# Performance work log

Measured on AMD Instinct MI355X. Metric: run time of the kernel, lower is better.

Reference implementation:

```python
import jax, jax.numpy as jnp
import numpy as np

B_SZ, SEQ, H, P = 4, 8192, 512, 256


def _s5(x, lam_re, lam_im, log_dt, b_re, b_im, c_re, c_im, d):
    """Single-direction S5 diagonal SSM. x: [B,L,H] -> y: [B,L,H]."""
    lam = lam_re + 1j * lam_im                      # [P] complex diagonal A
    dt = jnp.exp(log_dt)                            # [P] ZOH timestep
    a_bar = jnp.exp(lam * dt)                       # [P] discretized A
    b_bar = ((a_bar - 1.0) / lam)[:, None] * (b_re + 1j * b_im)  # [P,H]
    bu = jnp.einsum('blh,ph->blp', x.astype(b_bar.dtype), b_bar)  # [B,L,P]
    a_el = jnp.broadcast_to(a_bar, bu.shape)        # time-invariant A per step

    def comb(e1, e2):  # associative combine for linear recurrence
        a1, s1 = e1
        a2, s2 = e2
        return (a1 * a2, a2 * s1 + s2)

    _, states = jax.lax.associative_scan(comb, (a_el, bu), axis=1)  # [B,L,P]
    c = c_re + 1j * c_im                            # [H,P]
    return jnp.einsum('blp,hp->blh', states, c).real + x * d


def setup_inputs() -> dict:
    key = jax.random.key(0)
    ks = jax.random.split(key, 10)
    return {
        'x': jax.random.normal(ks[0], (B_SZ, SEQ, H), dtype=jnp.float32),
        'Lambda_re': -0.1 - 0.5 * jax.random.uniform(ks[1], (2, P), dtype=jnp.float32),
        'Lambda_im': jnp.pi * jax.random.normal(ks[2], (2, P), dtype=jnp.float32),
        'log_dt': jnp.log(0.001) + (jnp.log(0.1) - jnp.log(0.001)) * jax.random.uniform(ks[3], (2, P), dtype=jnp.float32),
        'B_re': jax.random.normal(ks[4], (2, P, H), dtype=jnp.float32) / np.sqrt(H),
        'B_im': jax.random.normal(ks[5], (2, P, H), dtype=jnp.float32) / np.sqrt(H),
        'C_re': jax.random.normal(ks[6], (2, H, P), dtype=jnp.float32) / np.sqrt(P),
        'C_im': jax.random.normal(ks[7], (2, H, P), dtype=jnp.float32) / np.sqrt(P),
        'D': jax.random.normal(ks[8], (2, H), dtype=jnp.float32),
    }


def reference(x, Lambda_re, Lambda_im, log_dt, B_re, B_im, C_re, C_im, D):
    # fwd(x) + flip(bwd(flip(x)))
    y_f = _s5(x, Lambda_re[0], Lambda_im[0], log_dt[0], B_re[0], B_im[0], C_re[0], C_im[0], D[0])
    x_r = x[:, ::-1]
    y_b = _s5(x_r, Lambda_re[1], Lambda_im[1], log_dt[1], B_re[1], B_im[1], C_re[1], C_im[1], D[1])[:, ::-1]
    return y_f + y_b
```

## Files before the change

kernel.cpp:

```cpp
#include <hip/hip_runtime.h>
#include <math.h>

typedef unsigned short ushort_t;
typedef __bf16 bf16x8 __attribute__((ext_vector_type(8)));
typedef ushort_t ushort8v __attribute__((ext_vector_type(8)));
typedef float f32x4 __attribute__((ext_vector_type(4)));

#define B_SZ   4
#define SEQ    8192
#define M_ROWS (B_SZ * SEQ)
#define CH     128
#define NC     (SEQ / CH)

__device__ __forceinline__ ushort_t f2bf(float f) {
    unsigned u = __float_as_uint(f);
    u = u + 0x7fffu + ((u >> 16) & 1u);
    return (ushort_t)(u >> 16);
}
__device__ __forceinline__ float bf2f(ushort_t b) {
    return __uint_as_float(((unsigned)b) << 16);
}

__device__ __forceinline__ void load16_lds(const void* g, void* l) {
    __builtin_amdgcn_global_load_lds(
        (const __attribute__((address_space(1))) unsigned int*)g,
        (__attribute__((address_space(3))) unsigned int*)l, 16, 0, 0);
}

__device__ __forceinline__ bf16x8 ldfrag(const ushort_t* p) {
    union { ushort8v u; bf16x8 b; } cv;
    cv.u = *(const ushort8v*)p;
    return cv.b;
}

__device__ __forceinline__ float2 cmul(float2 a, float2 b) {
    return make_float2(a.x * b.x - a.y * b.y, a.x * b.y + a.y * b.x);
}

__global__ void prepconv_kernel(const float* __restrict__ x,
                                ushort_t* __restrict__ X16,
                                const float* __restrict__ Lre,
                                const float* __restrict__ Lim,
                                const float* __restrict__ ldt,
                                const float* __restrict__ Bre,
                                const float* __restrict__ Bim,
                                const float* __restrict__ Cre,
                                const float* __restrict__ Cim,
                                float* __restrict__ abar,
                                float* __restrict__ apow,
                                float* __restrict__ PW,
                                ushort_t* __restrict__ Bmat,
                                ushort_t* __restrict__ Cmat) {
    int i = blockIdx.x * 256 + threadIdx.x;
    float4 v = ((const float4*)x)[i];
    ushort_t o[4] = {f2bf(v.x), f2bf(v.y), f2bf(v.z), f2bf(v.w)};
    *(uint2*)&X16[(size_t)i * 4] = *(const uint2*)o;

    if (blockIdx.x < 1024) {
        int idx = i;
        int h = idx & 511;
        int p = (idx >> 9) & 255;
        int d = idx >> 17;
        int ip = d * 256 + p;
        float lr = Lre[ip], li = Lim[ip];
        float dt = expf(ldt[ip]);
        float e   = expf(lr * dt);
        float ang = li * dt;
        float ar = e * cosf(ang), ai = e * sinf(ang);
        float nr = ar - 1.0f, ni = ai;
        float den = lr * lr + li * li;
        float cr = (nr * lr + ni * li) / den;
        float ci = (ni * lr - nr * li) / den;
        float br = Bre[idx], bi = Bim[idx];
        Bmat[(d * 512 + 2 * p) * 512 + h]     = f2bf(cr * br - ci * bi);
        Bmat[(d * 512 + 2 * p + 1) * 512 + h] = f2bf(cr * bi + ci * br);
        if (h == 0) {
            int oo = d * 512 + 2 * p;
            abar[oo] = ar;  abar[oo + 1] = ai;
            float eC = expf(lr * dt * (float)CH);
            float aC = ang * (float)CH;
            apow[oo] = eC * cosf(aC);  apow[oo + 1] = eC * sinf(aC);
            float2 a1 = make_float2(ar, ai);
            float2 a2 = cmul(a1, a1);
            float2 a4 = cmul(a2, a2);
            float2 a8 = cmul(a4, a4);
            float2 a16 = cmul(a8, a8);
            float2 a32 = cmul(a16, a16);
            float2 a64 = cmul(a32, a32);
            int q = d * 256 + p;
            PW[q * 8 + 0] = a1.x;  PW[q * 8 + 1] = a1.y;
            PW[q * 8 + 2] = a4.x;  PW[q * 8 + 3] = a4.y;
            PW[q * 8 + 4] = a16.x; PW[q * 8 + 5] = a16.y;
            PW[q * 8 + 6] = a64.x; PW[q * 8 + 7] = a64.y;
        }
        int p2 = idx & 255;
        int h2 = (idx >> 8) & 511;
        int d2 = idx >> 17;
        Cmat[h2 * 1024 + d2 * 512 + 2 * p2]     = f2bf(Cre[idx]);
        Cmat[h2 * 1024 + d2 * 512 + 2 * p2 + 1] = f2bf(-Cim[idx]);
    }
}

template<int EPI, int KD_, int NT>
__global__ __launch_bounds__(512, 4)
void gemm_bk32(const ushort_t* __restrict__ A, const ushort_t* __restrict__ Bm,
               ushort_t* __restrict__ Cb, float* __restrict__ Cf,
               const float* __restrict__ X, const float* __restrict__ Dv,
               const float* __restrict__ PW, float* __restrict__ CAR) {
    __shared__ char smem[49152];
    ushort_t (*shA)[4096] = (ushort_t(*)[4096])smem;
    ushort_t (*shB)[8192] = (ushort_t(*)[8192])(smem + 16384);
    constexpr int NKT = KD_ / 32;

    const int tid  = threadIdx.x;
    const int lane = tid & 63;
    const int wv   = tid >> 6;
    const int wr = wv >> 2, wc = wv & 3;
    const int l15 = lane & 15, lq = lane >> 4;

    const int lin = blockIdx.x;
    const int xcd = lin & 7;
    const int j   = lin >> 3;
    const int mt  = xcd * 32 + j / NT;
    const int nt  = j % NT;
    const int m0 = mt * 128;
    const int n0 = nt * 256;
    const int CN = NT * 256;

    f32x4 acc[4][4];
#pragma unroll
    for (int i = 0; i < 4; ++i)
#pragma unroll
        for (int jj = 0; jj < 4; ++jj)
            acc[i][jj] = (f32x4){0.f, 0.f, 0.f, 0.f};

    const int srA = wv * 16 + (lane >> 2);
    const int srB = wv * 32 + (lane >> 2);
    const int sck = (((lane & 3) ^ ((lane >> 3) & 3))) * 8;
    const ushort_t* Ag = A  + (size_t)(m0 + srA) * KD_ + sck;
    const ushort_t* Bg = Bm + (size_t)(n0 + srB) * KD_ + sck;

#define STAGE(t) do {                                                         \
        load16_lds(Ag + (size_t)(t) * 32, &shA[(t) & 1][wv * 512]);           \
        load16_lds(Bg + (size_t)(t) * 32, &shB[(t) & 1][wv * 1024]);          \
        load16_lds(Bg + (size_t)(t) * 32 + (size_t)16 * KD_,                  \
                   &shB[(t) & 1][wv * 1024 + 512]);                           \
    } while (0)

    const int rdoff = ((lq ^ ((l15 >> 1) & 3))) * 8;
    const int rdA = (wr * 64 + l15) * 32 + rdoff;
    const int rdB = (wc * 64 + l15) * 32 + rdoff;

    STAGE(0); STAGE(1);
    asm volatile("s_waitcnt vmcnt(3)" ::: "memory");
    __builtin_amdgcn_s_barrier();

#pragma unroll 2
    for (int kt = 0; kt < NKT; ++kt) {
        const int buf = kt & 1;
        bf16x8 af[4], bq[4];
#pragma unroll
        for (int mi = 0; mi < 4; ++mi)
            af[mi] = ldfrag(&shA[buf][rdA + mi * 512]);
#pragma unroll
        for (int ni = 0; ni < 4; ++ni)
            bq[ni] = ldfrag(&shB[buf][rdB + ni * 512]);
        __builtin_amdgcn_s_barrier();
        if (kt + 2 < NKT) STAGE(kt + 2);
        __builtin_amdgcn_s_setprio(1);
#pragma unroll
        for (int mi = 0; mi < 4; ++mi)
#pragma unroll
            for (int ni = 0; ni < 4; ++ni)
                acc[mi][ni] = __builtin_amdgcn_mfma_f32_16x16x32_bf16(
                    af[mi], bq[ni], acc[mi][ni], 0, 0, 0);
        __builtin_amdgcn_s_setprio(0);
        if (kt + 1 < NKT) {
            if (kt + 2 < NKT)
                asm volatile("s_waitcnt vmcnt(3)" ::: "memory");
            else
                asm volatile("s_waitcnt vmcnt(0)" ::: "memory");
            __builtin_amdgcn_s_barrier();
        }
    }
#undef STAGE

    asm volatile("s_waitcnt lgkmcnt(0)" ::: "memory");
    __builtin_amdgcn_s_barrier();

    const int rr = lane >> 2;
    const int cc = (lane & 3) * 16;

    if (EPI == 0) {
        ushort_t* ep = (ushort_t*)(smem + wv * 2304);
#pragma unroll
        for (int mi = 0; mi < 4; ++mi) {
#pragma unroll
            for (int ni = 0; ni < 4; ++ni)
#pragma unroll
                for (int r = 0; r < 4; ++r)
                    ep[(lq * 4 + r) * 72 + ni * 16 + l15] = f2bf(acc[mi][ni][r]);
            uint4 w0 = *(const uint4*)&ep[rr * 72 + cc];
            uint4 w1 = *(const uint4*)&ep[rr * 72 + cc + 8];
            const int rowg = m0 + wr * 64 + mi * 16 + rr;
            *(uint4*)&Cb[(size_t)rowg * CN + n0 + wc * 64 + cc]     = w0;
            *(uint4*)&Cb[(size_t)rowg * CN + n0 + wc * 64 + cc + 8] = w1;
        }
    } else {
        float* epf = (float*)(smem + wv * 4352);
        const int colbase = n0 + wc * 64 + cc;
        f32x4 dsv[4];
#pragma unroll
        for (int j4 = 0; j4 < 4; ++j4)
            dsv[j4] = *(const f32x4*)&Dv[colbase + j4 * 4]
                    + *(const f32x4*)&Dv[512 + colbase + j4 * 4];
#pragma unroll
        for (int mi = 0; mi < 4; ++mi) {
#pragma unroll
            for (int ni = 0; ni < 4; ++ni)
#pragma unroll
                for (int r = 0; r < 4; ++r)
                    epf[(lq * 4 + r) * 68 + ni * 16 + l15] = acc[mi][ni][r];
            const int rowg = m0 + wr * 64 + mi * 16 + rr;
            const size_t gb = (size_t)rowg * 512 + colbase;
#pragma unroll
            for (int j4 = 0; j4 < 4; ++j4) {
                f32x4 v  = *(const f32x4*)&epf[rr * 68 + cc + j4 * 4];
                f32x4 xv = *(const f32x4*)&X[gb + j4 * 4];
                v = v + xv * dsv[j4];
                *(f32x4*)&Cf[gb + j4 * 4] = v;
            }
        }
    }

    if (EPI == 0) {
        float* PLDS = (float*)(smem + 20480);
        const int dirq = ((n0 + wc * 64) >> 9) & 1;
        const bool evn = ((l15 & 1) == 0);
        float csA[4], cpA[4], a64x[4], a64y[4];

#define CACC(MI, R, CCo) do {                                                 \
            float vo = bf2f(f2bf(acc[MI][ni][R]));                            \
            float vp = __shfl_xor(vo, 1);                                     \
            float vr = evn ? vo : vp;                                         \
            float vi = evn ? vp : vo;                                         \
            wr_ = fmaf(CCo.x, vr, fmaf(-CCo.y, vi, wr_));                     \
            wi_ = fmaf(CCo.x, vi, fmaf(CCo.y, vr, wi_));                      \
        } while (0)
#define CSTEP(MI) do {                                                        \
            float wr_ = 0.f, wi_ = 0.f;                                       \
            CACC(MI, 0, c0); CACC(MI, 1, c1);                                 \
            CACC(MI, 2, c2); CACC(MI, 3, c3);                                 \
            float comp = evn ? (t16.x * wr_ - t16.y * wi_)                    \
                             : (t16.x * wi_ + t16.y * wr_);                   \
            csum += comp;                                                     \
            t16 = cmul(t16, A16);                                             \
        } while (0)

#pragma unroll
        for (int ni = 0; ni < 4; ++ni) {
            const int col = n0 + wc * 64 + ni * 16 + l15;
            const int q = col >> 1;
            float2 A1  = make_float2(PW[q * 8 + 0], PW[q * 8 + 1]);
            float2 A4  = make_float2(PW[q * 8 + 2], PW[q * 8 + 3]);
            float2 A16 = make_float2(PW[q * 8 + 4], PW[q * 8 + 5]);
            a64x[ni] = PW[q * 8 + 6]; a64y[ni] = PW[q * 8 + 7];
            const int lqp = dirq ? lq : 3 - lq;
            float2 A4_2 = cmul(A4, A4);
            float2 A4_3 = cmul(A4_2, A4);
            float2 P4 = (lqp == 0) ? make_float2(1.f, 0.f)
                       : (lqp == 1) ? A4
                       : (lqp == 2) ? A4_2 : A4_3;
            float2 c0, c1, c2, c3;
            if (dirq == 0) {
                c3 = P4; c2 = cmul(c3, A1); c1 = cmul(c2, A1); c0 = cmul(c1, A1);
            } else {
                c0 = P4; c1 = cmul(c0, A1); c2 = cmul(c1, A1); c3 = cmul(c2, A1);
            }
            float2 t16 = make_float2(1.f, 0.f);
            float csum = 0.f;
            if (dirq == 0) { CSTEP(3); CSTEP(2); CSTEP(1); CSTEP(0); }
            else           { CSTEP(0); CSTEP(1); CSTEP(2); CSTEP(3); }
            csum += __shfl_xor(csum, 16);
            csum += __shfl_xor(csum, 32);
            csA[ni] = csum;
            cpA[ni] = __shfl_xor(csum, 1);
            if (lq == 0)
                PLDS[wr * 256 + wc * 64 + ni * 16 + l15] = csum;
        }
        __builtin_amdgcn_s_barrier();
        if (wr == 0) {
#pragma unroll
            for (int ni = 0; ni < 4; ++ni) {
                const int cl = wc * 64 + ni * 16 + l15;
                float oth_same = PLDS[256 + cl];
                float oth_part = PLDS[256 + (cl ^ 1)];
                float own_re = evn ? csA[ni] : cpA[ni];
                float own_im = evn ? cpA[ni] : csA[ni];
                float oth_re = evn ? oth_same : oth_part;
                float oth_im = evn ? oth_part : oth_same;
                float Xre = dirq ? oth_re : own_re;
                float Xim = dirq ? oth_im : own_im;
                float Ysm = dirq ? csA[ni] : oth_same;
                float out = evn
                    ? fmaf(a64x[ni], Xre, fmaf(-a64y[ni], Xim, Ysm))
                    : fmaf(a64x[ni], Xim, fmaf( a64y[ni], Xre, Ysm));
                if (lq == 0)
                    CAR[(size_t)(m0 >> 7) * 1024 + n0 + cl] = out;
            }
        }
#undef CACC
#undef CSTEP
    }
}

__global__ __launch_bounds__(512)
void scan_fin2(ushort_t* __restrict__ S, const float* __restrict__ abar,
               const float* __restrict__ apow, const float* __restrict__ carry) {
    int b = blockIdx.x, c = blockIdx.y, t = threadIdx.x;
    int dir = t >> 8, p = t & 255;
    float ar = abar[dir * 512 + 2 * p], ai = abar[dir * 512 + 2 * p + 1];
    float pr = apow[dir * 512 + 2 * p], pi = apow[dir * 512 + 2 * p + 1];
    float sr = 0.f, si = 0.f;
    if (dir == 0) {
        for (int cc = 0; cc < c; ++cc) {
            int o = (b * NC + cc) * 1024 + 2 * p;
            float cr0 = carry[o], ci0 = carry[o + 1];
            float nr = fmaf(pr, sr, fmaf(-pi, si, cr0));
            float ni = fmaf(pr, si, fmaf(pi, sr, ci0));
            sr = nr; si = ni;
        }
    } else {
        for (int cc = NC - 1; cc > c; --cc) {
            int o = (b * NC + cc) * 1024 + 512 + 2 * p;
            float cr0 = carry[o], ci0 = carry[o + 1];
            float nr = fmaf(pr, sr, fmaf(-pi, si, cr0));
            float ni = fmaf(pr, si, fmaf(pi, sr, ci0));
            sr = nr; si = ni;
        }
    }
    ushort_t* base = S + ((size_t)b * SEQ + (size_t)c * CH) * 1024
                       + dir * 512 + 2 * p;
    for (int ii = 0; ii < CH; ++ii) {
        int i = dir ? (CH - 1 - ii) : ii;
        unsigned* addr = (unsigned*)(base + (size_t)i * 1024);
        unsigned u = *addr;
        float re = bf2f((ushort_t)(u & 0xffffu));
        float im = bf2f((ushort_t)(u >> 16));
        float nr = fmaf(ar, sr, fmaf(-ai, si, re));
        float ni = fmaf(ar, si, fmaf(ai, sr, im));
        sr = nr; si = ni;
        *addr = ((unsigned)f2bf(si) << 16) | (unsigned)f2bf(sr);
    }
}

extern "C" void kernel_launch(void* const* d_in, const int* in_sizes, int n_in,
                              void* d_out, int out_size, void* d_ws, size_t ws_size,
                              hipStream_t stream) {
    const float* x   = (const float*)d_in[0];
    const float* Lre = (const float*)d_in[1];
    const float* Lim = (const float*)d_in[2];
    const float* ldt = (const float*)d_in[3];
    const float* Bre = (const float*)d_in[4];
    const float* Bim = (const float*)d_in[5];
    const float* Cre = (const float*)d_in[6];
    const float* Cim = (const float*)d_in[7];
    const float* Dv  = (const float*)d_in[8];
    float* y = (float*)d_out;
    char* ws = (char*)d_ws;

    ushort_t* SB16 = (ushort_t*)(ws);
    ushort_t* X16  = (ushort_t*)(ws + 67108864);
    ushort_t* Bm16 = (ushort_t*)(ws + 100663296);
    ushort_t* Cm16 = (ushort_t*)(ws + 101711872);
    float* abar  = (float*)(ws + 102760448);
    float* apow  = (float*)(ws + 102764544);
    float* carry = (float*)d_out;
    float* PW    = (float*)((char*)d_out + 1048576);

    prepconv_kernel<<<16384, 256, 0, stream>>>(x, X16, Lre, Lim, ldt,
                                               Bre, Bim, Cre, Cim,
                                               abar, apow, PW, Bm16, Cm16);

    gemm_bk32<0, 512, 4><<<1024, 512, 0, stream>>>(X16, Bm16, SB16, nullptr,
                                                   nullptr, nullptr, PW, carry);

    dim3 gs(B_SZ, NC);
    scan_fin2<<<gs, 512, 0, stream>>>(SB16, abar, apow, carry);

    gemm_bk32<1, 1024, 2><<<512, 512, 0, stream>>>(SB16, Cm16, nullptr, y,
                                                   x, Dv, nullptr, nullptr);
}
```

Measured before the change: 279.8 us.

## Fuse x bf16 conversion into GEMM1 and fuse scan fixup into GEMM2

Drops the separate x-to-bf16 pass: GEMM1 now loads fp32 x from global, converts it in registers and writes it to LDS. Per-64-row chunk carries are emitted straight from GEMM1 without the cross-warp combine. A new kernel, one block per 64-row chunk, serially accumulates the carries, applies the intra-chunk scan in registers, stores the states to LDS and runs the C projection GEMM there with the D skip term. This removes the X16 round trip, the in-place scan's read-modify-write of SB, and one launch. The cost is a long serial carry loop per block (up to 127 steps), a 160KB LDS footprint that allows only one block per CU, and A-tile conversion work added to GEMM1.

```diff
diff --git a/kernel.cpp b/kernel.cpp
--- a/kernel.cpp
+++ b/kernel.cpp
@@ -37,80 +37,65 @@
     return make_float2(a.x * b.x - a.y * b.y, a.x * b.y + a.y * b.x);
 }
 
-__global__ void prepconv_kernel(const float* __restrict__ x,
-                                ushort_t* __restrict__ X16,
-                                const float* __restrict__ Lre,
-                                const float* __restrict__ Lim,
-                                const float* __restrict__ ldt,
-                                const float* __restrict__ Bre,
-                                const float* __restrict__ Bim,
-                                const float* __restrict__ Cre,
-                                const float* __restrict__ Cim,
-                                float* __restrict__ abar,
-                                float* __restrict__ apow,
-                                float* __restrict__ PW,
-                                ushort_t* __restrict__ Bmat,
-                                ushort_t* __restrict__ Cmat) {
-    int i = blockIdx.x * 256 + threadIdx.x;
-    float4 v = ((const float4*)x)[i];
-    ushort_t o[4] = {f2bf(v.x), f2bf(v.y), f2bf(v.z), f2bf(v.w)};
-    *(uint2*)&X16[(size_t)i * 4] = *(const uint2*)o;
-
-    if (blockIdx.x < 1024) {
-        int idx = i;
-        int h = idx & 511;
-        int p = (idx >> 9) & 255;
-        int d = idx >> 17;
-        int ip = d * 256 + p;
-        float lr = Lre[ip], li = Lim[ip];
-        float dt = expf(ldt[ip]);
-        float e   = expf(lr * dt);
-        float ang = li * dt;
-        float ar = e * cosf(ang), ai = e * sinf(ang);
-        float nr = ar - 1.0f, ni = ai;
-        float den = lr * lr + li * li;
-        float cr = (nr * lr + ni * li) / den;
-        float ci = (ni * lr - nr * li) / den;
-        float br = Bre[idx], bi = Bim[idx];
-        Bmat[(d * 512 + 2 * p) * 512 + h]     = f2bf(cr * br - ci * bi);
-        Bmat[(d * 512 + 2 * p + 1) * 512 + h] = f2bf(cr * bi + ci * br);
-        if (h == 0) {
-            int oo = d * 512 + 2 * p;
-            abar[oo] = ar;  abar[oo + 1] = ai;
-            float eC = expf(lr * dt * (float)CH);
-            float aC = ang * (float)CH;
-            apow[oo] = eC * cosf(aC);  apow[oo + 1] = eC * sinf(aC);
-            float2 a1 = make_float2(ar, ai);
-            float2 a2 = cmul(a1, a1);
-            float2 a4 = cmul(a2, a2);
-            float2 a8 = cmul(a4, a4);
-            float2 a16 = cmul(a8, a8);
-            float2 a32 = cmul(a16, a16);
-            float2 a64 = cmul(a32, a32);
-            int q = d * 256 + p;
-            PW[q * 8 + 0] = a1.x;  PW[q * 8 + 1] = a1.y;
-            PW[q * 8 + 2] = a4.x;  PW[q * 8 + 3] = a4.y;
-            PW[q * 8 + 4] = a16.x; PW[q * 8 + 5] = a16.y;
-            PW[q * 8 + 6] = a64.x; PW[q * 8 + 7] = a64.y;
-        }
-        int p2 = idx & 255;
-        int h2 = (idx >> 8) & 511;
-        int d2 = idx >> 17;
-        Cmat[h2 * 1024 + d2 * 512 + 2 * p2]     = f2bf(Cre[idx]);
-        Cmat[h2 * 1024 + d2 * 512 + 2 * p2 + 1] = f2bf(-Cim[idx]);
-    }
-}
-
-template<int EPI, int KD_, int NT>
+__global__ void prep_kernel(const float* __restrict__ Lre,
+                            const float* __restrict__ Lim,
+                            const float* __restrict__ ldt,
+                            const float* __restrict__ Bre,
+                            const float* __restrict__ Bim,
+                            const float* __restrict__ Cre,
+                            const float* __restrict__ Cim,
+                            float* __restrict__ abar,
+                            float* __restrict__ PW,
+                            ushort_t* __restrict__ Bmat,
+                            ushort_t* __restrict__ Cmat) {
+    int idx = blockIdx.x * 256 + threadIdx.x;
+    int h = idx & 511;
+    int p = (idx >> 9) & 255;
+    int d = idx >> 17;
+    int ip = d * 256 + p;
+    float lr = Lre[ip], li = Lim[ip];
+    float dt = expf(ldt[ip]);
+    float e   = expf(lr * dt);
+    float ang = li * dt;
+    float ar = e * cosf(ang), ai = e * sinf(ang);
+    float nr = ar - 1.0f, ni = ai;
+    float den = lr * lr + li * li;
+    float cr = (nr * lr + ni * li) / den;
+    float ci = (ni * lr - nr * li) / den;
+    float br = Bre[idx], bi = Bim[idx];
+    Bmat[(d * 512 + 2 * p) * 512 + h]     = f2bf(cr * br - ci * bi);
+    Bmat[(d * 512 + 2 * p + 1) * 512 + h] = f2bf(cr * bi + ci * br);
+    if (h == 0) {
+        int oo = d * 512 + 2 * p;
+        abar[oo] = ar;  abar[oo + 1] = ai;
+        float2 a1 = make_float2(ar, ai);
+        float2 a2 = cmul(a1, a1);
+        float2 a4 = cmul(a2, a2);
+        float2 a8 = cmul(a4, a4);
+        float2 a16 = cmul(a8, a8);
+        float2 a32 = cmul(a16, a16);
+        float2 a64 = cmul(a32, a32);
+        int q = d * 256 + p;
+        PW[q * 8 + 0] = a1.x;  PW[q * 8 + 1] = a1.y;
+        PW[q * 8 + 2] = a4.x;  PW[q * 8 + 3] = a4.y;
+        PW[q * 8 + 4] = a16.x; PW[q * 8 + 5] = a16.y;
+        PW[q * 8 + 6] = a64.x; PW[q * 8 + 7] = a64.y;
+    }
+    int p2 = idx & 255;
+    int h2 = (idx >> 8) & 511;
+    int d2 = idx >> 17;
+    Cmat[h2 * 1024 + d2 * 512 + 2 * p2]     = f2bf(Cre[idx]);
+    Cmat[h2 * 1024 + d2 * 512 + 2 * p2 + 1] = f2bf(-Cim[idx]);
+}
+
 __global__ __launch_bounds__(512, 4)
-void gemm_bk32(const ushort_t* __restrict__ A, const ushort_t* __restrict__ Bm,
-               ushort_t* __restrict__ Cb, float* __restrict__ Cf,
-               const float* __restrict__ X, const float* __restrict__ Dv,
-               const float* __restrict__ PW, float* __restrict__ CAR) {
+void gemm1_kernel(const float* __restrict__ Xf, const ushort_t* __restrict__ Bm,
+                  ushort_t* __restrict__ Cb, const float* __restrict__ PW,
+                  float* __restrict__ CAR) {
     __shared__ char smem[49152];
     ushort_t (*shA)[4096] = (ushort_t(*)[4096])smem;
     ushort_t (*shB)[8192] = (ushort_t(*)[8192])(smem + 16384);
-    constexpr int NKT = KD_ / 32;
+    constexpr int KD_ = 512, NT = 4, NKT = 16;
 
     const int tid  = threadIdx.x;
     const int lane = tid & 63;
@@ -134,14 +119,25 @@
         for (int jj = 0; jj < 4; ++jj)
             acc[i][jj] = (f32x4){0.f, 0.f, 0.f, 0.f};
 
-    const int srA = wv * 16 + (lane >> 2);
+    const int arow = tid >> 2;
+    const int ac   = tid & 3;
+    const float* Axg = Xf + (size_t)(m0 + arow) * KD_ + ac * 8;
+    const int awoff = arow * 64 + ((ac ^ ((arow >> 1) & 3)) * 16);
+
     const int srB = wv * 32 + (lane >> 2);
     const int sck = (((lane & 3) ^ ((lane >> 3) & 3))) * 8;
-    const ushort_t* Ag = A  + (size_t)(m0 + srA) * KD_ + sck;
     const ushort_t* Bg = Bm + (size_t)(n0 + srB) * KD_ + sck;
 
-#define STAGE(t) do {                                                         \
-        load16_lds(Ag + (size_t)(t) * 32, &shA[(t) & 1][wv * 512]);           \
+    float4 aLo, aHi;
+#define GLB_A(t) do { aLo = *(const float4*)(Axg + (size_t)(t) * 32);         \
+                      aHi = *(const float4*)(Axg + (size_t)(t) * 32 + 4);     \
+                 } while (0)
+#define WRITE_A(t) do {                                                       \
+        ushort_t tmp[8] = {f2bf(aLo.x), f2bf(aLo.y), f2bf(aLo.z), f2bf(aLo.w),\
+                           f2bf(aHi.x), f2bf(aHi.y), f2bf(aHi.z), f2bf(aHi.w)};\
+        *(uint4*)((char*)&shA[(t) & 1][0] + awoff) = *(const uint4*)tmp;      \
+    } while (0)
+#define STAGE_B(t) do {                                                       \
         load16_lds(Bg + (size_t)(t) * 32, &shB[(t) & 1][wv * 1024]);          \
         load16_lds(Bg + (size_t)(t) * 32 + (size_t)16 * KD_,                  \
                    &shB[(t) & 1][wv * 1024 + 512]);                           \
@@ -151,8 +147,11 @@
     const int rdA = (wr * 64 + l15) * 32 + rdoff;
     const int rdB = (wc * 64 + l15) * 32 + rdoff;
 
-    STAGE(0); STAGE(1);
-    asm volatile("s_waitcnt vmcnt(3)" ::: "memory");
+    GLB_A(0);
+    STAGE_B(0); STAGE_B(1);
+    WRITE_A(0);
+    asm volatile("s_waitcnt vmcnt(2)" ::: "memory");
+    asm volatile("s_waitcnt lgkmcnt(0)" ::: "memory");
     __builtin_amdgcn_s_barrier();
 
 #pragma unroll 2
@@ -165,8 +164,13 @@
 #pragma unroll
         for (int ni = 0; ni < 4; ++ni)
             bq[ni] = ldfrag(&shB[buf][rdB + ni * 512]);
+        if (kt + 1 < NKT) GLB_A(kt + 1);
         __builtin_amdgcn_s_barrier();
-        if (kt + 2 < NKT) STAGE(kt + 2);
+        if (kt + 2 < NKT) STAGE_B(kt + 2);
+        if (kt + 1 < NKT) {
+            WRITE_A(kt + 1);
+            asm volatile("s_waitcnt vmcnt(2)" ::: "memory");
+        }
         __builtin_amdgcn_s_setprio(1);
 #pragma unroll
         for (int mi = 0; mi < 4; ++mi)
@@ -176,22 +180,20 @@
                     af[mi], bq[ni], acc[mi][ni], 0, 0, 0);
         __builtin_amdgcn_s_setprio(0);
         if (kt + 1 < NKT) {
-            if (kt + 2 < NKT)
-                asm volatile("s_waitcnt vmcnt(3)" ::: "memory");
-            else
-                asm volatile("s_waitcnt vmcnt(0)" ::: "memory");
+            asm volatile("s_waitcnt lgkmcnt(0)" ::: "memory");
             __builtin_amdgcn_s_barrier();
         }
     }
-#undef STAGE
+#undef GLB_A
+#undef WRITE_A
+#undef STAGE_B
 
     asm volatile("s_waitcnt lgkmcnt(0)" ::: "memory");
     __builtin_amdgcn_s_barrier();
 
     const int rr = lane >> 2;
     const int cc = (lane & 3) * 16;
-
-    if (EPI == 0) {
+    {
         ushort_t* ep = (ushort_t*)(smem + wv * 2304);
 #pragma unroll
         for (int mi = 0; mi < 4; ++mi) {
@@ -206,38 +208,11 @@
             *(uint4*)&Cb[(size_t)rowg * CN + n0 + wc * 64 + cc]     = w0;
             *(uint4*)&Cb[(size_t)rowg * CN + n0 + wc * 64 + cc + 8] = w1;
         }
-    } else {
-        float* epf = (float*)(smem + wv * 4352);
-        const int colbase = n0 + wc * 64 + cc;
-        f32x4 dsv[4];
-#pragma unroll
-        for (int j4 = 0; j4 < 4; ++j4)
-            dsv[j4] = *(const f32x4*)&Dv[colbase + j4 * 4]
-                    + *(const f32x4*)&Dv[512 + colbase + j4 * 4];
-#pragma unroll
-        for (int mi = 0; mi < 4; ++mi) {
-#pragma unroll
-            for (int ni = 0; ni < 4; ++ni)
-#pragma unroll
-                for (int r = 0; r < 4; ++r)
-                    epf[(lq * 4 + r) * 68 + ni * 16 + l15] = acc[mi][ni][r];
-            const int rowg = m0 + wr * 64 + mi * 16 + rr;
-            const size_t gb = (size_t)rowg * 512 + colbase;
-#pragma unroll
-            for (int j4 = 0; j4 < 4; ++j4) {
-                f32x4 v  = *(const f32x4*)&epf[rr * 68 + cc + j4 * 4];
-                f32x4 xv = *(const f32x4*)&X[gb + j4 * 4];
-                v = v + xv * dsv[j4];
-                *(f32x4*)&Cf[gb + j4 * 4] = v;
-            }
-        }
-    }
-
-    if (EPI == 0) {
-        float* PLDS = (float*)(smem + 20480);
+    }
+
+    {
         const int dirq = ((n0 + wc * 64) >> 9) & 1;
         const bool evn = ((l15 & 1) == 0);
-        float csA[4], cpA[4], a64x[4], a64y[4];
 
 #define CACC(MI, R, CCo) do {                                                 \
             float vo = bf2f(f2bf(acc[MI][ni][R]));                            \
@@ -264,7 +239,6 @@
             float2 A1  = make_float2(PW[q * 8 + 0], PW[q * 8 + 1]);
             float2 A4  = make_float2(PW[q * 8 + 2], PW[q * 8 + 3]);
             float2 A16 = make_float2(PW[q * 8 + 4], PW[q * 8 + 5]);
-            a64x[ni] = PW[q * 8 + 6]; a64y[ni] = PW[q * 8 + 7];
             const int lqp = dirq ? lq : 3 - lq;
             float2 A4_2 = cmul(A4, A4);
             float2 A4_3 = cmul(A4_2, A4);
@@ -283,31 +257,8 @@
             else           { CSTEP(0); CSTEP(1); CSTEP(2); CSTEP(3); }
             csum += __shfl_xor(csum, 16);
             csum += __shfl_xor(csum, 32);
-            csA[ni] = csum;
-            cpA[ni] = __shfl_xor(csum, 1);
             if (lq == 0)
-                PLDS[wr * 256 + wc * 64 + ni * 16 + l15] = csum;
-        }
-        __builtin_amdgcn_s_barrier();
-        if (wr == 0) {
-#pragma unroll
-            for (int ni = 0; ni < 4; ++ni) {
-                const int cl = wc * 64 + ni * 16 + l15;
-                float oth_same = PLDS[256 + cl];
-                float oth_part = PLDS[256 + (cl ^ 1)];
-                float own_re = evn ? csA[ni] : cpA[ni];
-                float own_im = evn ? cpA[ni] : csA[ni];
-                float oth_re = evn ? oth_same : oth_part;
-                float oth_im = evn ? oth_part : oth_same;
-                float Xre = dirq ? oth_re : own_re;
-                float Xim = dirq ? oth_im : own_im;
-                float Ysm = dirq ? csA[ni] : oth_same;
-                float out = evn
-                    ? fmaf(a64x[ni], Xre, fmaf(-a64y[ni], Xim, Ysm))
-                    : fmaf(a64x[ni], Xim, fmaf( a64y[ni], Xre, Ysm));
-                if (lq == 0)
-                    CAR[(size_t)(m0 >> 7) * 1024 + n0 + cl] = out;
-            }
+                CAR[(size_t)((m0 >> 6) + wr) * 1024 + col] = csum;
         }
 #undef CACC
 #undef CSTEP
@@ -315,42 +266,151 @@
 }
 
 __global__ __launch_bounds__(512)
-void scan_fin2(ushort_t* __restrict__ S, const float* __restrict__ abar,
-               const float* __restrict__ apow, const float* __restrict__ carry) {
-    int b = blockIdx.x, c = blockIdx.y, t = threadIdx.x;
-    int dir = t >> 8, p = t & 255;
-    float ar = abar[dir * 512 + 2 * p], ai = abar[dir * 512 + 2 * p + 1];
-    float pr = apow[dir * 512 + 2 * p], pi = apow[dir * 512 + 2 * p + 1];
-    float sr = 0.f, si = 0.f;
-    if (dir == 0) {
-        for (int cc = 0; cc < c; ++cc) {
-            int o = (b * NC + cc) * 1024 + 2 * p;
-            float cr0 = carry[o], ci0 = carry[o + 1];
-            float nr = fmaf(pr, sr, fmaf(-pi, si, cr0));
-            float ni = fmaf(pr, si, fmaf(pi, sr, ci0));
-            sr = nr; si = ni;
-        }
-    } else {
-        for (int cc = NC - 1; cc > c; --cc) {
-            int o = (b * NC + cc) * 1024 + 512 + 2 * p;
-            float cr0 = carry[o], ci0 = carry[o + 1];
-            float nr = fmaf(pr, sr, fmaf(-pi, si, cr0));
-            float ni = fmaf(pr, si, fmaf(pi, sr, ci0));
-            sr = nr; si = ni;
-        }
-    }
-    ushort_t* base = S + ((size_t)b * SEQ + (size_t)c * CH) * 1024
-                       + dir * 512 + 2 * p;
-    for (int ii = 0; ii < CH; ++ii) {
-        int i = dir ? (CH - 1 - ii) : ii;
-        unsigned* addr = (unsigned*)(base + (size_t)i * 1024);
-        unsigned u = *addr;
-        float re = bf2f((ushort_t)(u & 0xffffu));
-        float im = bf2f((ushort_t)(u >> 16));
-        float nr = fmaf(ar, sr, fmaf(-ai, si, re));
-        float ni = fmaf(ar, si, fmaf(ai, sr, im));
-        sr = nr; si = ni;
-        *addr = ((unsigned)f2bf(si) << 16) | (unsigned)f2bf(sr);
+void scan_gemm2_kernel(const ushort_t* __restrict__ SB,
+                       const ushort_t* __restrict__ Cm,
+                       const float* __restrict__ abar,
+                       const float* __restrict__ CAR,
+                       const float* __restrict__ Xf,
+                       const float* __restrict__ Dv,
+                       float* __restrict__ Y) {
+    __shared__ char smem[163840];
+    const int tid = threadIdx.x;
+    const int blk = blockIdx.x;
+    const int gm0 = blk * 64;
+    const int bidx = blk >> 7;
+    const int hb   = blk & 127;
+
+    {
+        const int dir = tid >> 8, p = tid & 255;
+        const int col = dir * 512 + 2 * p;
+        const int q   = dir * 256 + p;
+        float2 a1 = *(const float2*)&abar[col];
+        float2 a2 = cmul(a1, a1), a4 = cmul(a2, a2), a8 = cmul(a4, a4);
+        float2 a16 = cmul(a8, a8), a32 = cmul(a16, a16), a64 = cmul(a32, a32);
+
+        float sr = 0.f, si = 0.f;
+        if (dir == 0) {
+            for (int hc = 0; hc < hb; ++hc) {
+                float2 c = *(const float2*)&CAR[(size_t)(bidx * 128 + hc) * 1024 + col];
+                float nr = fmaf(a64.x, sr, fmaf(-a64.y, si, c.x));
+                float ni = fmaf(a64.x, si, fmaf( a64.y, sr, c.y));
+                sr = nr; si = ni;
+            }
+        } else {
+            for (int hc = 127; hc > hb; --hc) {
+                float2 c = *(const float2*)&CAR[(size_t)(bidx * 128 + hc) * 1024 + col];
+                float nr = fmaf(a64.x, sr, fmaf(-a64.y, si, c.x));
+                float ni = fmaf(a64.x, si, fmaf( a64.y, sr, c.y));
+                sr = nr; si = ni;
+            }
+        }
+
+        const unsigned* SBu = (const unsigned*)SB;
+        unsigned u[64];
+#pragma unroll
+        for (int i = 0; i < 64; ++i)
+            u[i] = SBu[(size_t)(gm0 + i) * 512 + q];
+
+        if (dir == 0) {
+#pragma unroll
+            for (int i = 0; i < 64; ++i) {
+                float re = bf2f((ushort_t)(u[i] & 0xffffu));
+                float im = bf2f((ushort_t)(u[i] >> 16));
+                float nr = fmaf(a1.x, sr, fmaf(-a1.y, si, re));
+                float ni = fmaf(a1.x, si, fmaf( a1.y, sr, im));
+                sr = nr; si = ni;
+                u[i] = ((unsigned)f2bf(si) << 16) | (unsigned)f2bf(sr);
+            }
+        } else {
+#pragma unroll
+            for (int i = 63; i >= 0; --i) {
+                float re = bf2f((ushort_t)(u[i] & 0xffffu));
+                float im = bf2f((ushort_t)(u[i] >> 16));
+                float nr = fmaf(a1.x, sr, fmaf(-a1.y, si, re));
+                float ni = fmaf(a1.x, si, fmaf( a1.y, sr, im));
+                sr = nr; si = ni;
+                u[i] = ((unsigned)f2bf(si) << 16) | (unsigned)f2bf(sr);
+            }
+        }
+#pragma unroll
+        for (int i = 0; i < 64; ++i)
+            *(unsigned*)(smem + ((i * 2048 + col * 2) ^ ((i & 7) << 4))) = u[i];
+    }
+    __syncthreads();
+
+    const int lane = tid & 63, wv = tid >> 6;
+    const int l15 = lane & 15, lq = lane >> 4;
+    constexpr int NKT2 = 32;
+    char* Blds = smem + 131072;
+
+    f32x4 acc[4][4];
+#pragma unroll
+    for (int i = 0; i < 4; ++i)
+#pragma unroll
+        for (int jj = 0; jj < 4; ++jj)
+            acc[i][jj] = (f32x4){0.f, 0.f, 0.f, 0.f};
+
+    const ushort_t* Bg = Cm + (size_t)tid * 1024;
+    uint4 bA[4], bB[4];
+#define BGLB(dst, t) do { _Pragma("unroll")                                   \
+        for (int c = 0; c < 4; ++c)                                           \
+            dst[c] = *(const uint4*)(Bg + (size_t)(t) * 32 + c * 8);          \
+    } while (0)
+#define BWRITE(src) do { _Pragma("unroll")                                    \
+        for (int c = 0; c < 4; ++c)                                           \
+            *(uint4*)(Blds + c * 8192 + tid * 16) = src[c];                   \
+    } while (0)
+
+    BGLB(bA, 0); BGLB(bB, 1);
+    BWRITE(bA);
+    asm volatile("s_waitcnt lgkmcnt(0)" ::: "memory");
+    __builtin_amdgcn_s_barrier();
+
+    const int axk = (l15 & 7) << 4;
+    for (int t = 0; t < NKT2; ++t) {
+        if (t + 2 < NKT2) { if ((t & 1) == 0) BGLB(bA, t + 2); else BGLB(bB, t + 2); }
+        bf16x8 af[4], bf[4];
+#pragma unroll
+        for (int mi = 0; mi < 4; ++mi) {
+            const int row = mi * 16 + l15;
+            af[mi] = ldfrag((const ushort_t*)(smem +
+                        ((row * 2048 + t * 64 + lq * 16) ^ axk)));
+        }
+#pragma unroll
+        for (int ni = 0; ni < 4; ++ni)
+            bf[ni] = ldfrag((const ushort_t*)(Blds + lq * 8192 +
+                        (wv * 64 + ni * 16 + l15) * 16));
+        asm volatile("s_waitcnt lgkmcnt(0)" ::: "memory");
+        __builtin_amdgcn_s_barrier();
+        if (t + 1 < NKT2) { if ((t & 1) == 0) BWRITE(bB); else BWRITE(bA); }
+        __builtin_amdgcn_s_setprio(1);
+#pragma unroll
+        for (int mi = 0; mi < 4; ++mi)
+#pragma unroll
+            for (int ni = 0; ni < 4; ++ni)
+                acc[mi][ni] = __builtin_amdgcn_mfma_f32_16x16x32_bf16(
+                    af[mi], bf[ni], acc[mi][ni], 0, 0, 0);
+        __builtin_amdgcn_s_setprio(0);
+        if (t + 1 < NKT2) {
+            asm volatile("s_waitcnt lgkmcnt(0)" ::: "memory");
+            __builtin_amdgcn_s_barrier();
+        }
+    }
+#undef BGLB
+#undef BWRITE
+
+#pragma unroll
+    for (int ni = 0; ni < 4; ++ni) {
+        const int colY = wv * 64 + ni * 16 + l15;
+        const float dsum = Dv[colY] + Dv[512 + colY];
+#pragma unroll
+        for (int mi = 0; mi < 4; ++mi)
+#pragma unroll
+            for (int r = 0; r < 4; ++r) {
+                const int row = gm0 + mi * 16 + lq * 4 + r;
+                const size_t idx = (size_t)row * 512 + colY;
+                Y[idx] = acc[mi][ni][r] + Xf[idx] * dsum;
+            }
     }
 }
 
@@ -369,25 +429,18 @@
     float* y = (float*)d_out;
     char* ws = (char*)d_ws;
 
-    ushort_t* SB16 = (ushort_t*)(ws);
-    ushort_t* X16  = (ushort_t*)(ws + 67108864);
-    ushort_t* Bm16 = (ushort_t*)(ws + 100663296);
-    ushort_t* Cm16 = (ushort_t*)(ws + 101711872);
-    float* abar  = (float*)(ws + 102760448);
-    float* apow  = (float*)(ws + 102764544);
-    float* carry = (float*)d_out;
-    float* PW    = (float*)((char*)d_out + 1048576);
-
-    prepconv_kernel<<<16384, 256, 0, stream>>>(x, X16, Lre, Lim, ldt,
-                                               Bre, Bim, Cre, Cim,
-                                               abar, apow, PW, Bm16, Cm16);
-
-    gemm_bk32<0, 512, 4><<<1024, 512, 0, stream>>>(X16, Bm16, SB16, nullptr,
-                                                   nullptr, nullptr, PW, carry);
-
-    dim3 gs(B_SZ, NC);
-    scan_fin2<<<gs, 512, 0, stream>>>(SB16, abar, apow, carry);
-
-    gemm_bk32<1, 1024, 2><<<512, 512, 0, stream>>>(SB16, Cm16, nullptr, y,
-                                                   x, Dv, nullptr, nullptr);
-}
+    ushort_t* SB16  = (ushort_t*)(ws);
+    float*    CAR64 = (float*)(ws + 67108864);
+    ushort_t* Bm16  = (ushort_t*)(ws + 100663296);
+    ushort_t* Cm16  = (ushort_t*)(ws + 101711872);
+    float*    abar  = (float*)(ws + 102760448);
+    float*    PW    = (float*)d_out;
+
+    prep_kernel<<<1024, 256, 0, stream>>>(Lre, Lim, ldt, Bre, Bim, Cre, Cim,
+                                          abar, PW, Bm16, Cm16);
+
+    gemm1_kernel<<<1024, 512, 0, stream>>>(x, Bm16, SB16, PW, CAR64);
+
+    scan_gemm2_kernel<<<512, 512, 0, stream>>>(SB16, Cm16, abar, CAR64,
+                                               x, Dv, y);
+}
```

Result: slower. 432.3 us (+54.5%).
